# Performance work log

Measured on AMD Instinct MI355X. Metric: run time of the kernel, lower is better.

Reference implementation:

```python
import jax, jax.numpy as jnp
import numpy as np

B, S, I, C, P = 64, 14, 32, 10, 4   # batch, spatial, in-caps/pos, classes, pose size
ROUTINGS = 3
EPS = 1e-9


def setup_inputs() -> dict:
    key = jax.random.key(0)
    k1, k2, k3, k4, k5 = jax.random.split(key, 5)
    return {
        "inputs_pose": jax.random.normal(k1, (B, S, S, I, P, P), jnp.float32),
        "inputs_activation": jax.random.uniform(k2, (B, S, S, I), jnp.float32),
        "w": jax.random.normal(k3, (1, I, C, P, P), jnp.float32),
        "beta_v": jax.random.normal(k4, (1, C), jnp.float32) * 0.1,
        "beta_a": jax.random.normal(k5, (1, C), jnp.float32) * 0.1,
    }


def _em_routing(votes, i_act, beta_v, beta_a, routings):
    # votes: [B, N, C, 16], i_act: [B, N]
    Bn, N, Cc, D = votes.shape
    rr = jnp.full((Bn, N, Cc, 1), 1.0 / Cc, votes.dtype)  # uniform init assignments
    bv = beta_v.reshape(1, 1, Cc, 1)
    ba = beta_a.reshape(1, 1, Cc, 1)
    it_min, it_max = 1.0, min(float(routings), 3.0)  # inverse-temperature schedule
    o_mean = o_act = None
    for it in range(routings):
        inv_temp = it_min + (it_max - it_min) * it / max(1.0, routings - 1.0)
        # --- M step ---
        rr_p = rr * i_act[:, :, None, None]                        # [B,N,C,1]
        rr_sum = jnp.sum(rr_p, axis=1, keepdims=True)              # [B,1,C,1]
        o_mean = jnp.sum(rr_p * votes, axis=1, keepdims=True) / rr_sum   # [B,1,C,16]
        o_var = jnp.sum(rr_p * jnp.square(votes - o_mean), axis=1, keepdims=True) / rr_sum
        o_stdv = jnp.sqrt(o_var)                                   # [B,1,C,16]
        cost = jnp.sum((bv + jnp.log(o_stdv + EPS)) * rr_sum, axis=-1, keepdims=True)  # [B,1,C,1]
        o_act = jax.nn.sigmoid(inv_temp * (ba - cost))             # [B,1,C,1]
        # --- E step (skipped on last iteration) ---
        if it < routings - 1:
            logp = (-jnp.sum(jnp.square(votes - o_mean) / (2.0 * jnp.square(o_stdv) + EPS),
                             axis=-1, keepdims=True)
                    - jnp.sum(jnp.log(o_stdv + EPS), axis=-1, keepdims=True))  # [B,N,C,1]
            zz = jnp.log(o_act + EPS) + logp
            rr = jax.nn.softmax(zz, axis=2)
    return o_mean[:, 0], o_act[:, 0, :, 0]  # [B,C,16], [B,C]


def reference(inputs_pose, inputs_activation, w, beta_v, beta_a):
    # mat_transform: votes[b,h,w,i,c] = pose[b,h,w,i] @ W[i,c]   (4x4 matmuls)
    votes = jnp.einsum('bhwipq,icqr->bhwicpr', inputs_pose, w[0])
    votes = votes.reshape(B, S, S, I, C, P * P)
    # coordinate addition: scaled (row+0.5)/S onto pose element 0, col onto element 1
    coord = (jnp.arange(S, dtype=votes.dtype) + 0.5) / S
    votes = votes.at[..., 0].add(coord[None, :, None, None, None])
    votes = votes.at[..., 1].add(coord[None, None, :, None, None])
    votes = votes.reshape(B, S * S * I, C, P * P)
    acts = inputs_activation.reshape(B, S * S * I)
    o_mean, o_act = _em_routing(votes, acts, beta_v, beta_a, ROUTINGS)
    pose = o_mean.reshape(B, C, P, P)
    return pose, o_act
```

## Files before the change

kernel.cpp:

```cpp
#include <hip/hip_runtime.h>
#include <math.h>

#define Bsz 64
#define Ssz 14
#define Isz 32
#define Csz 10
#define Dsz 16
#define Nsz (Ssz*Ssz*Isz)
#define EPSF 1e-9f

#define CH   640
#define NCH  10
#define MCH  3136
#define PST  36
#define MST  72

template<int CTRL, int RMASK>
__device__ __forceinline__ float dpp_add(float x) {
    int y = __builtin_amdgcn_update_dpp(0, __float_as_int(x), CTRL, RMASK, 0xf, true);
    return x + __int_as_float(y);
}
__device__ __forceinline__ float wave_sum64(float x) {
    x = dpp_add<0x111, 0xf>(x);
    x = dpp_add<0x112, 0xf>(x);
    x = dpp_add<0x114, 0xf>(x);
    x = dpp_add<0x118, 0xf>(x);
    x = dpp_add<0x142, 0xa>(x);
    x = dpp_add<0x143, 0xc>(x);
    return x;
}

__global__ __launch_bounds__(640) void mom_kernel(
    const float* __restrict__ pose,
    const float* __restrict__ act,
    float* __restrict__ partM)
{
    const int b = blockIdx.x, mch = blockIdx.y;
    const int tid = threadIdx.x, lane = tid & 63;

    __shared__ float Macc[32][73];

    float s[69];
#pragma unroll
    for (int j = 0; j < 69; ++j) s[j] = 0.f;

    const float* poseb = pose + (size_t)b*Nsz*Dsz;
    const float* actb  = act  + (size_t)b*Nsz;
    const int base = mch*MCH;

    for (int k = 0; k < MCH; k += 640) {
        const int nl = k + tid;
        if (nl < MCH) {
            const int n = base + nl;
            const float4* pp = reinterpret_cast<const float4*>(poseb + (size_t)n*Dsz);
            float4 a0 = pp[0], a1 = pp[1], a2 = pp[2], a3 = pp[3];
            float p[16] = {a0.x,a0.y,a0.z,a0.w, a1.x,a1.y,a1.z,a1.w,
                           a2.x,a2.y,a2.z,a2.w, a3.x,a3.y,a3.z,a3.w};
            const int hw = n >> 5;
            const int wc = hw % Ssz, hr = hw / Ssz;
            const float chh = (hr+0.5f)*(1.0f/Ssz), cww = (wc+0.5f)*(1.0f/Ssz);
            const float wgt = actb[n]*(1.0f/Csz);
            s[0] += wgt;
            float wp[16];
#pragma unroll
            for (int j = 0; j < 16; ++j) { wp[j] = wgt*p[j]; s[1+j] += wp[j]; }
            int t = 17;
#pragma unroll
            for (int pr = 0; pr < 4; ++pr)
#pragma unroll
                for (int k1 = 0; k1 < 4; ++k1)
#pragma unroll
                    for (int k2 = k1; k2 < 4; ++k2)
                        s[t++] += wp[pr*4+k1]*p[pr*4+k2];
            const float wch = wgt*chh, wcw = wgt*cww;
#pragma unroll
            for (int j = 0; j < 4; ++j) { s[57+j] += wch*p[j]; s[61+j] += wcw*p[j]; }
            s[65] += wch; s[66] += wcw; s[67] += wch*chh; s[68] += wcw*cww;
        }
    }
#pragma unroll
    for (int j = 0; j < 69; ++j) s[j] += __shfl_xor(s[j], 32);

    for (int t = tid; t < 32*73; t += 640) (&Macc[0][0])[t] = 0.f;
    __syncthreads();
    if (lane < 32) {
#pragma unroll
        for (int j = 0; j < 69; ++j) atomicAdd(&Macc[lane][j], s[j]);
    }
    __syncthreads();
    float* ob = partM + (size_t)(b*2 + mch)*32*MST;
    for (int t = tid; t < 32*MST; t += 640) {
        const int i = t / MST, j = t - i*MST;
        ob[t] = (j < 69) ? Macc[i][j] : 0.f;
    }
}

__global__ __launch_bounds__(256) void fin0_kernel(
    const float* __restrict__ partM,
    const float* __restrict__ w,
    const float* __restrict__ beta_v, const float* __restrict__ beta_a,
    float* __restrict__ prm, float inv_temp)
{
    const int b = blockIdx.x, tid = threadIdx.x;
    __shared__ float Mr[32][73];
    __shared__ float Ws[Isz*Csz*Dsz];
    __shared__ float pm[Csz][16], pg[Csz][16], pl[Csz][16];
    __shared__ float s0sh;

    const float* p0 = partM + (size_t)(b*2 + 0)*32*MST;
    const float* p1 = partM + (size_t)(b*2 + 1)*32*MST;
    for (int t = tid; t < 32*MST; t += 256) {
        const int i = t / MST, j = t - i*MST;
        Mr[i][j] = p0[t] + p1[t];
    }
    for (int t = tid; t < Isz*Csz*Dsz; t += 256) Ws[t] = w[t];
    __syncthreads();

    if (tid < Csz*Dsz) {
        const int c = tid >> 4, d = tid & 15, pr = d >> 2, r = d & 3;
        float S0 = 0.f, S1 = 0.f, S2 = 0.f;
        for (int i = 0; i < 32; ++i) {
            const float* Wi = Ws + (i*Csz + c)*Dsz;
            const float* Mi = Mr[i];
            S0 += Mi[0];
            const float w0 = Wi[0*4+r], w1 = Wi[1*4+r], w2 = Wi[2*4+r], w3 = Wi[3*4+r];
            const float* M1 = Mi + 1 + pr*4;
            S1 += w0*M1[0] + w1*M1[1] + w2*M1[2] + w3*M1[3];
            const float* Q = Mi + 17 + pr*10;
            S2 += w0*w0*Q[0] + w1*w1*Q[4] + w2*w2*Q[7] + w3*w3*Q[9]
                + 2.f*(w0*w1*Q[1] + w0*w2*Q[2] + w0*w3*Q[3]
                     + w1*w2*Q[5] + w1*w3*Q[6] + w2*w3*Q[8]);
            if (d == 0) {
                S1 += Mi[65];
                S2 += 2.f*(w0*Mi[57] + w1*Mi[58] + w2*Mi[59] + w3*Mi[60]) + Mi[67];
            } else if (d == 1) {
                S1 += Mi[66];
                S2 += 2.f*(w0*Mi[61] + w1*Mi[62] + w2*Mi[63] + w3*Mi[64]) + Mi[68];
            }
        }
        const float mean = S1 / S0;
        const float var = fmaxf(S2/S0 - mean*mean, 0.f);
        pm[c][d] = mean;
        pg[c][d] = 1.f/(2.f*var + EPSF);
        pl[c][d] = __logf(sqrtf(var) + EPSF);
        if (tid == 0) s0sh = S0;
    }
    __syncthreads();
    if (tid < Csz) {
        const int c = tid;
        float sumlog = 0.f;
#pragma unroll
        for (int d = 0; d < 16; ++d) sumlog += pl[c][d];
        const float cost = s0sh*(16.f*beta_v[c] + sumlog);
        const float oact = 1.f/(1.f + __expf(-inv_temp*(beta_a[c] - cost)));
        const float K = __logf(oact + EPSF) - sumlog;
        float* o = prm + (size_t)(b*Csz + c)*PST;
#pragma unroll
        for (int d = 0; d < 16; ++d) { o[d] = pm[c][d]; o[16+d] = pg[c][d]; }
        o[32] = K;
    }
}

__global__ __launch_bounds__(640) void em_kernel(
    const float* __restrict__ pose, const float* __restrict__ act,
    const float* __restrict__ w, const float* __restrict__ prm,
    float* __restrict__ partC)
{
    const int b = blockIdx.x, chunk = blockIdx.y;
    const int tid = threadIdx.x, wv = tid >> 6, lane = tid & 63;

    __shared__ float Wm[Csz][Isz*17];
    __shared__ float rr[Csz][CH];

    for (int t = tid; t < Csz*Isz*Dsz; t += 640) {
        const int cc = t >> 9, rem = t & 511, i = rem >> 4, q = rem & 15;
        Wm[cc][i*17 + q] = w[(i*Csz + cc)*Dsz + q];
    }
    __syncthreads();

    const int base = chunk*CH;
    const float* poseb = pose + (size_t)b*Nsz*Dsz;

    {
        const int n = base + tid;
        if (n < Nsz) {
            const float4* pp = reinterpret_cast<const float4*>(poseb + (size_t)n*Dsz);
            float4 a0 = pp[0], a1 = pp[1], a2 = pp[2], a3 = pp[3];
            float p[16] = {a0.x,a0.y,a0.z,a0.w, a1.x,a1.y,a1.z,a1.w,
                           a2.x,a2.y,a2.z,a2.w, a3.x,a3.y,a3.z,a3.w};
            const int i = tid & 31;
            const int hw = n >> 5;
            const int wc = hw % Ssz, hr = hw / Ssz;
            const float chh = (hr+0.5f)*(1.0f/Ssz), cww = (wc+0.5f)*(1.0f/Ssz);
            const float a = act[(size_t)b*Nsz + n];
            float zz[Csz];
#pragma unroll
            for (int c = 0; c < Csz; ++c) {
                const float* __restrict__ Wi = &Wm[c][i*17];
                const float* __restrict__ pg = prm + (size_t)(b*Csz + c)*PST;
                float quad = 0.f;
#pragma unroll
                for (int pr = 0; pr < 4; ++pr) {
#pragma unroll
                    for (int r = 0; r < 4; ++r) {
                        float vv = p[pr*4+0]*Wi[0*4+r] + p[pr*4+1]*Wi[1*4+r]
                                 + p[pr*4+2]*Wi[2*4+r] + p[pr*4+3]*Wi[3*4+r];
                        if (pr == 0 && r == 0) vv += chh;
                        if (pr == 0 && r == 1) vv += cww;
                        const int d = pr*4 + r;
                        const float dv = vv - pg[d];
                        quad += dv*dv*pg[16+d];
                    }
                }
                zz[c] = pg[32] - quad;
            }
            float zmax = zz[0];
#pragma unroll
            for (int c = 1; c < Csz; ++c) zmax = fmaxf(zmax, zz[c]);
            float zsum = 0.f;
#pragma unroll
            for (int c = 0; c < Csz; ++c) { zz[c] = __expf(zz[c] - zmax); zsum += zz[c]; }
            const float sc = __fdividef(a, zsum);
#pragma unroll
            for (int c = 0; c < Csz; ++c) rr[c][tid] = zz[c]*sc;
        }
    }
    __syncthreads();

    const int c = wv;
    float W16[16];
#pragma unroll
    for (int j = 0; j < 16; ++j) W16[j] = Wm[c][(lane & 31)*17 + j];

    float s0 = 0.f, s1[16], s2[16];
#pragma unroll
    for (int d = 0; d < 16; ++d) { s1[d] = 0.f; s2[d] = 0.f; }

    for (int k = 0; k < CH; k += 64) {
        const int nl = k + lane;
        const int n = base + nl;
        if (n < Nsz) {
            const float4* pp = reinterpret_cast<const float4*>(poseb + (size_t)n*Dsz);
            const int hw = n >> 5;
            const int wc2 = hw % Ssz, hr2 = hw / Ssz;
            const float chh = (hr2+0.5f)*(1.0f/Ssz), cww = (wc2+0.5f)*(1.0f/Ssz);
            const float wgt = rr[c][nl];
            s0 += wgt;
#pragma unroll
            for (int pr = 0; pr < 4; ++pr) {
                const float4 pv = pp[pr];
#pragma unroll
                for (int r = 0; r < 4; ++r) {
                    float vv = pv.x*W16[0*4+r] + pv.y*W16[1*4+r]
                             + pv.z*W16[2*4+r] + pv.w*W16[3*4+r];
                    if (pr == 0 && r == 0) vv += chh;
                    if (pr == 0 && r == 1) vv += cww;
                    const float wvv = wgt*vv;
                    s1[pr*4+r] += wvv;
                    s2[pr*4+r] += wvv*vv;
                }
            }
        }
    }
    s0 = wave_sum64(s0);
#pragma unroll
    for (int d = 0; d < 16; ++d) { s1[d] = wave_sum64(s1[d]); s2[d] = wave_sum64(s2[d]); }
    if (lane == 63) {
        const int bc = b*Csz + c;
        float* pt = partC + (size_t)chunk*33*(Bsz*Csz) + bc;
        pt[0] = s0;
#pragma unroll
        for (int d = 0; d < 16; ++d) {
            pt[(size_t)(1+d)*(Bsz*Csz)]  = s1[d];
            pt[(size_t)(17+d)*(Bsz*Csz)] = s2[d];
        }
    }
}

__global__ __launch_bounds__(64) void fin12_kernel(
    const float* __restrict__ partC, const float* __restrict__ beta_v,
    const float* __restrict__ beta_a, float* __restrict__ prm,
    float* __restrict__ out, float inv_temp)
{
    const int bc = blockIdx.x*64 + threadIdx.x;
    const int c = bc % Csz;
    float S[33];
#pragma unroll
    for (int j = 0; j < 33; ++j) S[j] = 0.f;
    for (int ch = 0; ch < NCH; ++ch) {
        const float* pb = partC + (size_t)ch*33*(Bsz*Csz) + bc;
#pragma unroll
        for (int j = 0; j < 33; ++j) S[j] += pb[(size_t)j*(Bsz*Csz)];
    }
    const float S0 = S[0], rS0 = 1.f/S0;
    float mean[16], gv[16];
    float sumlog = 0.f;
#pragma unroll
    for (int d = 0; d < 16; ++d) {
        const float mn = S[1+d]*rS0;
        const float var = fmaxf(S[17+d]*rS0 - mn*mn, 0.f);
        mean[d] = mn;
        gv[d] = 1.f/(2.f*var + EPSF);
        sumlog += __logf(sqrtf(var) + EPSF);
    }
    const float cost = S0*(16.f*beta_v[c] + sumlog);
    const float oact = 1.f/(1.f + __expf(-inv_temp*(beta_a[c] - cost)));
    if (out) {
#pragma unroll
        for (int d = 0; d < 16; ++d) out[(size_t)bc*16 + d] = mean[d];
        out[(size_t)Bsz*Csz*Dsz + bc] = oact;
    } else {
        const float K = __logf(oact + EPSF) - sumlog;
        float* o = prm + (size_t)bc*PST;
#pragma unroll
        for (int d = 0; d < 16; ++d) { o[d] = mean[d]; o[16+d] = gv[d]; }
        o[32] = K;
    }
}

extern "C" void kernel_launch(void* const* d_in, const int* in_sizes, int n_in,
                              void* d_out, int out_size, void* d_ws, size_t ws_size,
                              hipStream_t stream)
{
    const float* pose = (const float*)d_in[0];
    const float* act  = (const float*)d_in[1];
    const float* w    = (const float*)d_in[2];
    const float* bv   = (const float*)d_in[3];
    const float* ba   = (const float*)d_in[4];
    float* out = (float*)d_out;

    float* partM = (float*)d_ws;
    float* partC = partM;
    float* prmA  = partM + (size_t)Bsz*2*32*MST;
    float* prmB  = prmA + (size_t)Bsz*Csz*PST;

    mom_kernel  <<<dim3(Bsz, 2),   640, 0, stream>>>(pose, act, partM);
    fin0_kernel <<<Bsz,            256, 0, stream>>>(partM, w, bv, ba, prmA, 1.0f);
    em_kernel   <<<dim3(Bsz, NCH), 640, 0, stream>>>(pose, act, w, prmA, partC);
    fin12_kernel<<<(Bsz*Csz)/64,    64, 0, stream>>>(partC, bv, ba, prmB, nullptr, 2.0f);
    em_kernel   <<<dim3(Bsz, NCH), 640, 0, stream>>>(pose, act, w, prmB, partC);
    fin12_kernel<<<(Bsz*Csz)/64,    64, 0, stream>>>(partC, bv, ba, nullptr, out, 3.0f);
}
```

Baseline: 254.7 us.

## Fuse finalize steps into EM kernels and restructure E-step per class wave

Removes the separate fin0 and intermediate fin12 kernels by having each EM block recompute the per-(batch, class) parameters from the partial moments at its start. mom_kernel now atomically accumulates its two halves into a zeroed buffer, which needs an extra memset. The E-step is restructured so each wave handles one class with its W in registers and the parameters broadcast via readlane, writing logits to shared memory before a per-point softmax pass. Every block redundantly redoes the reduction and the parameter math, and the launch bounds raise the occupancy target, which may pressure registers.

```diff
diff --git a/kernel.cpp b/kernel.cpp
--- a/kernel.cpp
+++ b/kernel.cpp
@@ -12,8 +12,9 @@
 #define CH   640
 #define NCH  10
 #define MCH  3136
-#define PST  36
-#define MST  72
+#define MROW 72
+#define PRMS 36
+#define BC   (Bsz*Csz)
 
 template<int CTRL, int RMASK>
 __device__ __forceinline__ float dpp_add(float x) {
@@ -56,10 +57,9 @@
             float4 a0 = pp[0], a1 = pp[1], a2 = pp[2], a3 = pp[3];
             float p[16] = {a0.x,a0.y,a0.z,a0.w, a1.x,a1.y,a1.z,a1.w,
                            a2.x,a2.y,a2.z,a2.w, a3.x,a3.y,a3.z,a3.w};
-            const int hw = n >> 5;
-            const int wc = hw % Ssz, hr = hw / Ssz;
-            const float chh = (hr+0.5f)*(1.0f/Ssz), cww = (wc+0.5f)*(1.0f/Ssz);
-            const float wgt = actb[n]*(1.0f/Csz);
+            const int hw = n >> 5, wc = hw % Ssz, hr = hw / Ssz;
+            const float chh = (hr+0.5f)*(1.f/Ssz), cww = (wc+0.5f)*(1.f/Ssz);
+            const float wgt = actb[n]*(1.f/Csz);
             s[0] += wgt;
             float wp[16];
 #pragma unroll
@@ -88,176 +88,195 @@
         for (int j = 0; j < 69; ++j) atomicAdd(&Macc[lane][j], s[j]);
     }
     __syncthreads();
-    float* ob = partM + (size_t)(b*2 + mch)*32*MST;
-    for (int t = tid; t < 32*MST; t += 640) {
-        const int i = t / MST, j = t - i*MST;
-        ob[t] = (j < 69) ? Macc[i][j] : 0.f;
-    }
-}
-
-__global__ __launch_bounds__(256) void fin0_kernel(
-    const float* __restrict__ partM,
-    const float* __restrict__ w,
-    const float* __restrict__ beta_v, const float* __restrict__ beta_a,
-    float* __restrict__ prm, float inv_temp)
-{
-    const int b = blockIdx.x, tid = threadIdx.x;
-    __shared__ float Mr[32][73];
-    __shared__ float Ws[Isz*Csz*Dsz];
-    __shared__ float pm[Csz][16], pg[Csz][16], pl[Csz][16];
-    __shared__ float s0sh;
-
-    const float* p0 = partM + (size_t)(b*2 + 0)*32*MST;
-    const float* p1 = partM + (size_t)(b*2 + 1)*32*MST;
-    for (int t = tid; t < 32*MST; t += 256) {
-        const int i = t / MST, j = t - i*MST;
-        Mr[i][j] = p0[t] + p1[t];
-    }
-    for (int t = tid; t < Isz*Csz*Dsz; t += 256) Ws[t] = w[t];
-    __syncthreads();
-
-    if (tid < Csz*Dsz) {
-        const int c = tid >> 4, d = tid & 15, pr = d >> 2, r = d & 3;
-        float S0 = 0.f, S1 = 0.f, S2 = 0.f;
-        for (int i = 0; i < 32; ++i) {
-            const float* Wi = Ws + (i*Csz + c)*Dsz;
-            const float* Mi = Mr[i];
-            S0 += Mi[0];
-            const float w0 = Wi[0*4+r], w1 = Wi[1*4+r], w2 = Wi[2*4+r], w3 = Wi[3*4+r];
-            const float* M1 = Mi + 1 + pr*4;
-            S1 += w0*M1[0] + w1*M1[1] + w2*M1[2] + w3*M1[3];
-            const float* Q = Mi + 17 + pr*10;
-            S2 += w0*w0*Q[0] + w1*w1*Q[4] + w2*w2*Q[7] + w3*w3*Q[9]
-                + 2.f*(w0*w1*Q[1] + w0*w2*Q[2] + w0*w3*Q[3]
-                     + w1*w2*Q[5] + w1*w3*Q[6] + w2*w3*Q[8]);
-            if (d == 0) {
-                S1 += Mi[65];
-                S2 += 2.f*(w0*Mi[57] + w1*Mi[58] + w2*Mi[59] + w3*Mi[60]) + Mi[67];
-            } else if (d == 1) {
-                S1 += Mi[66];
-                S2 += 2.f*(w0*Mi[61] + w1*Mi[62] + w2*Mi[63] + w3*Mi[64]) + Mi[68];
-            }
-        }
-        const float mean = S1 / S0;
-        const float var = fmaxf(S2/S0 - mean*mean, 0.f);
-        pm[c][d] = mean;
-        pg[c][d] = 1.f/(2.f*var + EPSF);
-        pl[c][d] = __logf(sqrtf(var) + EPSF);
-        if (tid == 0) s0sh = S0;
-    }
-    __syncthreads();
-    if (tid < Csz) {
-        const int c = tid;
-        float sumlog = 0.f;
-#pragma unroll
-        for (int d = 0; d < 16; ++d) sumlog += pl[c][d];
-        const float cost = s0sh*(16.f*beta_v[c] + sumlog);
-        const float oact = 1.f/(1.f + __expf(-inv_temp*(beta_a[c] - cost)));
-        const float K = __logf(oact + EPSF) - sumlog;
-        float* o = prm + (size_t)(b*Csz + c)*PST;
-#pragma unroll
-        for (int d = 0; d < 16; ++d) { o[d] = pm[c][d]; o[16+d] = pg[c][d]; }
-        o[32] = K;
-    }
-}
-
-__global__ __launch_bounds__(640) void em_kernel(
+    for (int t = tid; t < 32*MROW; t += 640) {
+        const int i = t / MROW, j = t - i*MROW;
+        if (j < 69) atomicAdd(&partM[(size_t)b*(32*MROW) + t], Macc[i][j]);
+    }
+}
+
+template<bool FIRST>
+__global__ __launch_bounds__(640, 5) void em_kernel(
     const float* __restrict__ pose, const float* __restrict__ act,
-    const float* __restrict__ w, const float* __restrict__ prm,
-    float* __restrict__ partC)
+    const float* __restrict__ w, const float* __restrict__ beta_v,
+    const float* __restrict__ beta_a, const float* __restrict__ partIn,
+    float* __restrict__ partOut, float inv_temp_prev)
 {
     const int b = blockIdx.x, chunk = blockIdx.y;
-    const int tid = threadIdx.x, wv = tid >> 6, lane = tid & 63;
-
-    __shared__ float Wm[Csz][Isz*17];
-    __shared__ float rr[Csz][CH];
-
-    for (int t = tid; t < Csz*Isz*Dsz; t += 640) {
-        const int cc = t >> 9, rem = t & 511, i = rem >> 4, q = rem & 15;
-        Wm[cc][i*17 + q] = w[(i*Csz + cc)*Dsz + q];
-    }
-    __syncthreads();
+    const int tid = threadIdx.x, wv_ = tid >> 6, lane = tid & 63;
+
+    __shared__ float Wm[FIRST ? Csz*Isz*17 : 1];
+    __shared__ float U2[Csz*CH];
+    __shared__ float prm[Csz][PRMS];
+    __shared__ float pl[Csz*Dsz];
+    __shared__ float s0sh;
+
+    if (FIRST) {
+        for (int t = tid; t < Csz*Isz*Dsz; t += 640) {
+            const int cc = t >> 9, rem = t & 511, i = rem >> 4, q = rem & 15;
+            Wm[cc*(Isz*17) + i*17 + q] = w[(i*Csz + cc)*Dsz + q];
+        }
+        for (int t = tid; t < 32*MROW; t += 640) {
+            const int i = t / MROW, j = t - i*MROW;
+            U2[i*73 + j] = partIn[(size_t)b*(32*MROW) + t];
+        }
+    } else {
+        if (tid < Csz*33) {
+            const int c2 = tid / 33, j = tid - c2*33;
+            float sacc = 0.f;
+            const float* pb = partIn + (size_t)j*BC + b*Csz + c2;
+            for (int ch = 0; ch < NCH; ++ch) sacc += pb[(size_t)ch*33*BC];
+            U2[c2*34 + j] = sacc;
+        }
+    }
+    __syncthreads();
+
+    if (tid < Csz*Dsz) {
+        const int c = tid >> 4, d = tid & 15;
+        if (FIRST) {
+            const int pr = d >> 2, r = d & 3;
+            float S0 = 0.f, S1 = 0.f, S2 = 0.f;
+            for (int i = 0; i < 32; ++i) {
+                const float* Mi = U2 + i*73;
+                const float* Wi = Wm + c*(Isz*17) + i*17;
+                S0 += Mi[0];
+                const float w0 = Wi[r], w1 = Wi[4+r], w2 = Wi[8+r], w3 = Wi[12+r];
+                const float* M1 = Mi + 1 + pr*4;
+                S1 += w0*M1[0] + w1*M1[1] + w2*M1[2] + w3*M1[3];
+                const float* Q = Mi + 17 + pr*10;
+                S2 += w0*w0*Q[0] + w1*w1*Q[4] + w2*w2*Q[7] + w3*w3*Q[9]
+                    + 2.f*(w0*w1*Q[1] + w0*w2*Q[2] + w0*w3*Q[3]
+                         + w1*w2*Q[5] + w1*w3*Q[6] + w2*w3*Q[8]);
+                if (d == 0) {
+                    S1 += Mi[65];
+                    S2 += 2.f*(w0*Mi[57] + w1*Mi[58] + w2*Mi[59] + w3*Mi[60]) + Mi[67];
+                } else if (d == 1) {
+                    S1 += Mi[66];
+                    S2 += 2.f*(w0*Mi[61] + w1*Mi[62] + w2*Mi[63] + w3*Mi[64]) + Mi[68];
+                }
+            }
+            const float mean = S1 / S0;
+            const float var = fmaxf(S2/S0 - mean*mean, 0.f);
+            prm[c][d]    = mean;
+            prm[c][16+d] = 1.f/(2.f*var + EPSF);
+            pl[tid]      = __logf(sqrtf(var) + EPSF);
+            if (tid == 0) s0sh = S0;
+        } else {
+            const float S0 = U2[c*34];
+            const float mn = U2[c*34 + 1 + d] / S0;
+            const float var = fmaxf(U2[c*34 + 17 + d]/S0 - mn*mn, 0.f);
+            prm[c][d]    = mn;
+            prm[c][16+d] = 1.f/(2.f*var + EPSF);
+            pl[tid]      = __logf(sqrtf(var) + EPSF);
+        }
+    }
+    __syncthreads();
+    if (tid < Csz) {
+        float sumlog = 0.f;
+#pragma unroll
+        for (int d = 0; d < 16; ++d) sumlog += pl[tid*16 + d];
+        const float S0 = FIRST ? s0sh : U2[tid*34];
+        const float cost = S0*(16.f*beta_v[tid] + sumlog);
+        const float oact = 1.f/(1.f + __expf(-inv_temp_prev*(beta_a[tid] - cost)));
+        prm[tid][32] = __logf(oact + EPSF) - sumlog;
+    }
+    __syncthreads();
+
+    const int c = wv_;
+    float W16[16];
+    if (FIRST) {
+#pragma unroll
+        for (int j = 0; j < 16; ++j) W16[j] = Wm[c*(Isz*17) + (lane & 31)*17 + j];
+    } else {
+        const float4* wp = reinterpret_cast<const float4*>(
+            w + ((size_t)(lane & 31)*Csz + c)*Dsz);
+        float4 q0 = wp[0], q1 = wp[1], q2 = wp[2], q3 = wp[3];
+        W16[0]=q0.x; W16[1]=q0.y; W16[2]=q0.z; W16[3]=q0.w;
+        W16[4]=q1.x; W16[5]=q1.y; W16[6]=q1.z; W16[7]=q1.w;
+        W16[8]=q2.x; W16[9]=q2.y; W16[10]=q2.z; W16[11]=q2.w;
+        W16[12]=q3.x; W16[13]=q3.y; W16[14]=q3.z; W16[15]=q3.w;
+    }
+    const float pv = (lane < 33) ? prm[c][lane] : 0.f;
+    const int pvi = __float_as_int(pv);
+    float m_s[16], g_s[16];
+#pragma unroll
+    for (int d = 0; d < 16; ++d) {
+        m_s[d] = __int_as_float(__builtin_amdgcn_readlane(pvi, d));
+        g_s[d] = __int_as_float(__builtin_amdgcn_readlane(pvi, 16 + d));
+    }
+    const float K_s = __int_as_float(__builtin_amdgcn_readlane(pvi, 32));
 
     const int base = chunk*CH;
     const float* poseb = pose + (size_t)b*Nsz*Dsz;
 
-    {
-        const int n = base + tid;
+    for (int k = 0; k < CH; k += 64) {
+        const int n = base + k + lane;
         if (n < Nsz) {
             const float4* pp = reinterpret_cast<const float4*>(poseb + (size_t)n*Dsz);
             float4 a0 = pp[0], a1 = pp[1], a2 = pp[2], a3 = pp[3];
             float p[16] = {a0.x,a0.y,a0.z,a0.w, a1.x,a1.y,a1.z,a1.w,
                            a2.x,a2.y,a2.z,a2.w, a3.x,a3.y,a3.z,a3.w};
-            const int i = tid & 31;
-            const int hw = n >> 5;
-            const int wc = hw % Ssz, hr = hw / Ssz;
-            const float chh = (hr+0.5f)*(1.0f/Ssz), cww = (wc+0.5f)*(1.0f/Ssz);
-            const float a = act[(size_t)b*Nsz + n];
-            float zz[Csz];
-#pragma unroll
-            for (int c = 0; c < Csz; ++c) {
-                const float* __restrict__ Wi = &Wm[c][i*17];
-                const float* __restrict__ pg = prm + (size_t)(b*Csz + c)*PST;
-                float quad = 0.f;
-#pragma unroll
-                for (int pr = 0; pr < 4; ++pr) {
-#pragma unroll
-                    for (int r = 0; r < 4; ++r) {
-                        float vv = p[pr*4+0]*Wi[0*4+r] + p[pr*4+1]*Wi[1*4+r]
-                                 + p[pr*4+2]*Wi[2*4+r] + p[pr*4+3]*Wi[3*4+r];
-                        if (pr == 0 && r == 0) vv += chh;
-                        if (pr == 0 && r == 1) vv += cww;
-                        const int d = pr*4 + r;
-                        const float dv = vv - pg[d];
-                        quad += dv*dv*pg[16+d];
-                    }
+            const int hw = n >> 5, wc2 = hw % Ssz, hr2 = hw / Ssz;
+            const float chh = (hr2+0.5f)*(1.f/Ssz), cww = (wc2+0.5f)*(1.f/Ssz);
+            float quad = 0.f;
+#pragma unroll
+            for (int pr = 0; pr < 4; ++pr) {
+#pragma unroll
+                for (int r = 0; r < 4; ++r) {
+                    float vvv = p[pr*4]*W16[r] + p[pr*4+1]*W16[4+r]
+                              + p[pr*4+2]*W16[8+r] + p[pr*4+3]*W16[12+r];
+                    if (pr == 0 && r == 0) vvv += chh;
+                    if (pr == 0 && r == 1) vvv += cww;
+                    const float dv = vvv - m_s[pr*4+r];
+                    quad += dv*dv*g_s[pr*4+r];
                 }
-                zz[c] = pg[32] - quad;
             }
-            float zmax = zz[0];
-#pragma unroll
-            for (int c = 1; c < Csz; ++c) zmax = fmaxf(zmax, zz[c]);
+            U2[c*CH + k + lane] = K_s - quad;
+        }
+    }
+    __syncthreads();
+
+    {
+        const int n = base + tid;
+        if (n < Nsz) {
+            float z[Csz];
+#pragma unroll
+            for (int cc = 0; cc < Csz; ++cc) z[cc] = U2[cc*CH + tid];
+            float zmax = z[0];
+#pragma unroll
+            for (int cc = 1; cc < Csz; ++cc) zmax = fmaxf(zmax, z[cc]);
             float zsum = 0.f;
 #pragma unroll
-            for (int c = 0; c < Csz; ++c) { zz[c] = __expf(zz[c] - zmax); zsum += zz[c]; }
-            const float sc = __fdividef(a, zsum);
-#pragma unroll
-            for (int c = 0; c < Csz; ++c) rr[c][tid] = zz[c]*sc;
-        }
-    }
-    __syncthreads();
-
-    const int c = wv;
-    float W16[16];
-#pragma unroll
-    for (int j = 0; j < 16; ++j) W16[j] = Wm[c][(lane & 31)*17 + j];
+            for (int cc = 0; cc < Csz; ++cc) { z[cc] = __expf(z[cc] - zmax); zsum += z[cc]; }
+            const float sc = __fdividef(act[(size_t)b*Nsz + n], zsum);
+#pragma unroll
+            for (int cc = 0; cc < Csz; ++cc) U2[cc*CH + tid] = z[cc]*sc;
+        }
+    }
+    __syncthreads();
 
     float s0 = 0.f, s1[16], s2[16];
 #pragma unroll
     for (int d = 0; d < 16; ++d) { s1[d] = 0.f; s2[d] = 0.f; }
-
     for (int k = 0; k < CH; k += 64) {
-        const int nl = k + lane;
-        const int n = base + nl;
+        const int n = base + k + lane;
         if (n < Nsz) {
             const float4* pp = reinterpret_cast<const float4*>(poseb + (size_t)n*Dsz);
-            const int hw = n >> 5;
-            const int wc2 = hw % Ssz, hr2 = hw / Ssz;
-            const float chh = (hr2+0.5f)*(1.0f/Ssz), cww = (wc2+0.5f)*(1.0f/Ssz);
-            const float wgt = rr[c][nl];
+            const int hw = n >> 5, wc2 = hw % Ssz, hr2 = hw / Ssz;
+            const float chh = (hr2+0.5f)*(1.f/Ssz), cww = (wc2+0.5f)*(1.f/Ssz);
+            const float wgt = U2[c*CH + k + lane];
             s0 += wgt;
 #pragma unroll
             for (int pr = 0; pr < 4; ++pr) {
-                const float4 pv = pp[pr];
+                const float4 pvv = pp[pr];
 #pragma unroll
                 for (int r = 0; r < 4; ++r) {
-                    float vv = pv.x*W16[0*4+r] + pv.y*W16[1*4+r]
-                             + pv.z*W16[2*4+r] + pv.w*W16[3*4+r];
-                    if (pr == 0 && r == 0) vv += chh;
-                    if (pr == 0 && r == 1) vv += cww;
-                    const float wvv = wgt*vv;
+                    float vvv = pvv.x*W16[r] + pvv.y*W16[4+r]
+                              + pvv.z*W16[8+r] + pvv.w*W16[12+r];
+                    if (pr == 0 && r == 0) vvv += chh;
+                    if (pr == 0 && r == 1) vvv += cww;
+                    const float wvv = wgt*vvv;
                     s1[pr*4+r] += wvv;
-                    s2[pr*4+r] += wvv*vv;
+                    s2[pr*4+r] += wvv*vvv;
                 }
             }
         }
@@ -266,21 +285,19 @@
 #pragma unroll
     for (int d = 0; d < 16; ++d) { s1[d] = wave_sum64(s1[d]); s2[d] = wave_sum64(s2[d]); }
     if (lane == 63) {
-        const int bc = b*Csz + c;
-        float* pt = partC + (size_t)chunk*33*(Bsz*Csz) + bc;
+        float* pt = partOut + (size_t)chunk*33*BC + b*Csz + c;
         pt[0] = s0;
 #pragma unroll
         for (int d = 0; d < 16; ++d) {
-            pt[(size_t)(1+d)*(Bsz*Csz)]  = s1[d];
-            pt[(size_t)(17+d)*(Bsz*Csz)] = s2[d];
-        }
-    }
-}
-
-__global__ __launch_bounds__(64) void fin12_kernel(
+            pt[(size_t)(1+d)*BC]  = s1[d];
+            pt[(size_t)(17+d)*BC] = s2[d];
+        }
+    }
+}
+
+__global__ __launch_bounds__(64) void fin_kernel(
     const float* __restrict__ partC, const float* __restrict__ beta_v,
-    const float* __restrict__ beta_a, float* __restrict__ prm,
-    float* __restrict__ out, float inv_temp)
+    const float* __restrict__ beta_a, float* __restrict__ out, float inv_temp)
 {
     const int bc = blockIdx.x*64 + threadIdx.x;
     const int c = bc % Csz;
@@ -288,40 +305,28 @@
 #pragma unroll
     for (int j = 0; j < 33; ++j) S[j] = 0.f;
     for (int ch = 0; ch < NCH; ++ch) {
-        const float* pb = partC + (size_t)ch*33*(Bsz*Csz) + bc;
-#pragma unroll
-        for (int j = 0; j < 33; ++j) S[j] += pb[(size_t)j*(Bsz*Csz)];
+        const float* pb = partC + (size_t)ch*33*BC + bc;
+#pragma unroll
+        for (int j = 0; j < 33; ++j) S[j] += pb[(size_t)j*BC];
     }
     const float S0 = S[0], rS0 = 1.f/S0;
-    float mean[16], gv[16];
     float sumlog = 0.f;
 #pragma unroll
     for (int d = 0; d < 16; ++d) {
         const float mn = S[1+d]*rS0;
         const float var = fmaxf(S[17+d]*rS0 - mn*mn, 0.f);
-        mean[d] = mn;
-        gv[d] = 1.f/(2.f*var + EPSF);
+        out[(size_t)bc*Dsz + d] = mn;
         sumlog += __logf(sqrtf(var) + EPSF);
     }
     const float cost = S0*(16.f*beta_v[c] + sumlog);
-    const float oact = 1.f/(1.f + __expf(-inv_temp*(beta_a[c] - cost)));
-    if (out) {
-#pragma unroll
-        for (int d = 0; d < 16; ++d) out[(size_t)bc*16 + d] = mean[d];
-        out[(size_t)Bsz*Csz*Dsz + bc] = oact;
-    } else {
-        const float K = __logf(oact + EPSF) - sumlog;
-        float* o = prm + (size_t)bc*PST;
-#pragma unroll
-        for (int d = 0; d < 16; ++d) { o[d] = mean[d]; o[16+d] = gv[d]; }
-        o[32] = K;
-    }
+    out[(size_t)Bsz*Csz*Dsz + bc] = 1.f/(1.f + __expf(-inv_temp*(beta_a[c] - cost)));
 }
 
 extern "C" void kernel_launch(void* const* d_in, const int* in_sizes, int n_in,
                               void* d_out, int out_size, void* d_ws, size_t ws_size,
                               hipStream_t stream)
 {
+    (void)in_sizes; (void)n_in; (void)out_size; (void)ws_size;
     const float* pose = (const float*)d_in[0];
     const float* act  = (const float*)d_in[1];
     const float* w    = (const float*)d_in[2];
@@ -329,15 +334,15 @@
     const float* ba   = (const float*)d_in[4];
     float* out = (float*)d_out;
 
-    float* partM = (float*)d_ws;
-    float* partC = partM;
-    float* prmA  = partM + (size_t)Bsz*2*32*MST;
-    float* prmB  = prmA + (size_t)Bsz*Csz*PST;
-
-    mom_kernel  <<<dim3(Bsz, 2),   640, 0, stream>>>(pose, act, partM);
-    fin0_kernel <<<Bsz,            256, 0, stream>>>(partM, w, bv, ba, prmA, 1.0f);
-    em_kernel   <<<dim3(Bsz, NCH), 640, 0, stream>>>(pose, act, w, prmA, partC);
-    fin12_kernel<<<(Bsz*Csz)/64,    64, 0, stream>>>(partC, bv, ba, prmB, nullptr, 2.0f);
-    em_kernel   <<<dim3(Bsz, NCH), 640, 0, stream>>>(pose, act, w, prmB, partC);
-    fin12_kernel<<<(Bsz*Csz)/64,    64, 0, stream>>>(partC, bv, ba, nullptr, out, 3.0f);
-}
+    float* regA = (float*)d_ws;
+    float* regB = regA + (size_t)NCH*33*BC;
+    float* partM  = regA;
+    float* partC  = regB;
+    float* partC2 = regA;
+
+    hipMemsetAsync(partM, 0, (size_t)Bsz*32*MROW*sizeof(float), stream);
+    mom_kernel      <<<dim3(Bsz, 2),   640, 0, stream>>>(pose, act, partM);
+    em_kernel<true> <<<dim3(Bsz, NCH), 640, 0, stream>>>(pose, act, w, bv, ba, partM, partC, 1.0f);
+    em_kernel<false><<<dim3(Bsz, NCH), 640, 0, stream>>>(pose, act, w, bv, ba, partC, partC2, 2.0f);
+    fin_kernel      <<<NCH,             64, 0, stream>>>(partC2, bv, ba, out, 3.0f);
+}
```

Measured after the change: 277.0 us. +8.8%, slower.

## Fuse moment accumulation with first M-step and parallelize finalize kernels

Applied to the files above, without the earlier changes.

Merges the moment-accumulation kernel and the first M-step finalize into one kernel per batch, which removes a launch and the partM round trip through global memory. The grid shrinks from 128 to 64 blocks, so each block now scans all N positions. The finalize kernel is reworked to run one 64-thread block per (batch, class), with the partial sums laid out contiguously per (b,c), so each thread reduces one statistic across the chunks and a shuffle reduction forms the log-sum. The trade-off is lower parallelism in the first kernel, which on a 256-CU part may lengthen that phase in exchange for the saved launch.

```diff
diff --git a/kernel.cpp b/kernel.cpp
--- a/kernel.cpp
+++ b/kernel.cpp
@@ -11,9 +11,9 @@
 
 #define CH   640
 #define NCH  10
-#define MCH  3136
 #define PST  36
-#define MST  72
+#define BC   (Bsz*Csz)
+#define CPL  (BC*33)
 
 template<int CTRL, int RMASK>
 __device__ __forceinline__ float dpp_add(float x) {
@@ -30,100 +30,80 @@
     return x;
 }
 
-__global__ __launch_bounds__(640) void mom_kernel(
+__global__ __launch_bounds__(640, 3) void momfin0_kernel(
     const float* __restrict__ pose,
     const float* __restrict__ act,
-    float* __restrict__ partM)
+    const float* __restrict__ w,
+    const float* __restrict__ beta_v,
+    const float* __restrict__ beta_a,
+    float* __restrict__ prmOut)
 {
-    const int b = blockIdx.x, mch = blockIdx.y;
+    const int b = blockIdx.x;
     const int tid = threadIdx.x, lane = tid & 63;
 
     __shared__ float Macc[32][73];
-
-    float s[69];
-#pragma unroll
-    for (int j = 0; j < 69; ++j) s[j] = 0.f;
+    __shared__ float U[3*640];
+    __shared__ float pl[Csz*Dsz];
+    __shared__ float sv[Csz];
+
+    for (int t = tid; t < 32*73; t += 640) (&Macc[0][0])[t] = 0.f;
+    __syncthreads();
 
     const float* poseb = pose + (size_t)b*Nsz*Dsz;
     const float* actb  = act  + (size_t)b*Nsz;
-    const int base = mch*MCH;
-
-    for (int k = 0; k < MCH; k += 640) {
-        const int nl = k + tid;
-        if (nl < MCH) {
-            const int n = base + nl;
-            const float4* pp = reinterpret_cast<const float4*>(poseb + (size_t)n*Dsz);
-            float4 a0 = pp[0], a1 = pp[1], a2 = pp[2], a3 = pp[3];
-            float p[16] = {a0.x,a0.y,a0.z,a0.w, a1.x,a1.y,a1.z,a1.w,
-                           a2.x,a2.y,a2.z,a2.w, a3.x,a3.y,a3.z,a3.w};
-            const int hw = n >> 5;
-            const int wc = hw % Ssz, hr = hw / Ssz;
-            const float chh = (hr+0.5f)*(1.0f/Ssz), cww = (wc+0.5f)*(1.0f/Ssz);
-            const float wgt = actb[n]*(1.0f/Csz);
-            s[0] += wgt;
-            float wp[16];
-#pragma unroll
-            for (int j = 0; j < 16; ++j) { wp[j] = wgt*p[j]; s[1+j] += wp[j]; }
-            int t = 17;
-#pragma unroll
-            for (int pr = 0; pr < 4; ++pr)
-#pragma unroll
-                for (int k1 = 0; k1 < 4; ++k1)
-#pragma unroll
-                    for (int k2 = k1; k2 < 4; ++k2)
-                        s[t++] += wp[pr*4+k1]*p[pr*4+k2];
-            const float wch = wgt*chh, wcw = wgt*cww;
-#pragma unroll
-            for (int j = 0; j < 4; ++j) { s[57+j] += wch*p[j]; s[61+j] += wcw*p[j]; }
-            s[65] += wch; s[66] += wcw; s[67] += wch*chh; s[68] += wcw*cww;
-        }
-    }
-#pragma unroll
-    for (int j = 0; j < 69; ++j) s[j] += __shfl_xor(s[j], 32);
-
-    for (int t = tid; t < 32*73; t += 640) (&Macc[0][0])[t] = 0.f;
+
+    {
+        float s[69];
+#pragma unroll
+        for (int j = 0; j < 69; ++j) s[j] = 0.f;
+        for (int k = 0; k < Nsz; k += CH) {
+            const int n = k + tid;
+            if (n < Nsz) {
+                const float4* pp = reinterpret_cast<const float4*>(poseb + (size_t)n*Dsz);
+                float4 a0 = pp[0], a1 = pp[1], a2 = pp[2], a3 = pp[3];
+                float p[16] = {a0.x,a0.y,a0.z,a0.w, a1.x,a1.y,a1.z,a1.w,
+                               a2.x,a2.y,a2.z,a2.w, a3.x,a3.y,a3.z,a3.w};
+                const int hw = n >> 5, wc = hw % Ssz, hr = hw / Ssz;
+                const float chh = (hr+0.5f)*(1.f/Ssz), cww = (wc+0.5f)*(1.f/Ssz);
+                const float wgt = actb[n]*(1.f/Csz);
+                s[0] += wgt;
+                float wp[16];
+#pragma unroll
+                for (int j = 0; j < 16; ++j) { wp[j] = wgt*p[j]; s[1+j] += wp[j]; }
+                int t = 17;
+#pragma unroll
+                for (int pr = 0; pr < 4; ++pr)
+#pragma unroll
+                    for (int k1 = 0; k1 < 4; ++k1)
+#pragma unroll
+                        for (int k2 = k1; k2 < 4; ++k2)
+                            s[t++] += wp[pr*4+k1]*p[pr*4+k2];
+                const float wch = wgt*chh, wcw = wgt*cww;
+#pragma unroll
+                for (int j = 0; j < 4; ++j) { s[57+j] += wch*p[j]; s[61+j] += wcw*p[j]; }
+                s[65] += wch; s[66] += wcw; s[67] += wch*chh; s[68] += wcw*cww;
+            }
+        }
+#pragma unroll
+        for (int j = 0; j < 69; ++j) s[j] += __shfl_xor(s[j], 32);
+        if (lane < 32) {
+#pragma unroll
+            for (int j = 0; j < 69; ++j) atomicAdd(&Macc[lane][j], s[j]);
+        }
+    }
     __syncthreads();
-    if (lane < 32) {
-#pragma unroll
-        for (int j = 0; j < 69; ++j) atomicAdd(&Macc[lane][j], s[j]);
-    }
-    __syncthreads();
-    float* ob = partM + (size_t)(b*2 + mch)*32*MST;
-    for (int t = tid; t < 32*MST; t += 640) {
-        const int i = t / MST, j = t - i*MST;
-        ob[t] = (j < 69) ? Macc[i][j] : 0.f;
-    }
-}
-
-__global__ __launch_bounds__(256) void fin0_kernel(
-    const float* __restrict__ partM,
-    const float* __restrict__ w,
-    const float* __restrict__ beta_v, const float* __restrict__ beta_a,
-    float* __restrict__ prm, float inv_temp)
-{
-    const int b = blockIdx.x, tid = threadIdx.x;
-    __shared__ float Mr[32][73];
-    __shared__ float Ws[Isz*Csz*Dsz];
-    __shared__ float pm[Csz][16], pg[Csz][16], pl[Csz][16];
-    __shared__ float s0sh;
-
-    const float* p0 = partM + (size_t)(b*2 + 0)*32*MST;
-    const float* p1 = partM + (size_t)(b*2 + 1)*32*MST;
-    for (int t = tid; t < 32*MST; t += 256) {
-        const int i = t / MST, j = t - i*MST;
-        Mr[i][j] = p0[t] + p1[t];
-    }
-    for (int t = tid; t < Isz*Csz*Dsz; t += 256) Ws[t] = w[t];
-    __syncthreads();
-
-    if (tid < Csz*Dsz) {
-        const int c = tid >> 4, d = tid & 15, pr = d >> 2, r = d & 3;
+
+    {
+        const int c = tid >> 6, d = (tid >> 2) & 15, g = tid & 3;
+        const int pr = d >> 2, r = d & 3;
         float S0 = 0.f, S1 = 0.f, S2 = 0.f;
-        for (int i = 0; i < 32; ++i) {
-            const float* Wi = Ws + (i*Csz + c)*Dsz;
-            const float* Mi = Mr[i];
+#pragma unroll
+        for (int ii = 0; ii < 8; ++ii) {
+            const int i = g*8 + ii;
+            const float* Mi = Macc[i];
+            const float* Wi = w + ((size_t)i*Csz + c)*Dsz;
             S0 += Mi[0];
-            const float w0 = Wi[0*4+r], w1 = Wi[1*4+r], w2 = Wi[2*4+r], w3 = Wi[3*4+r];
+            const float w0 = Wi[r], w1 = Wi[4+r], w2 = Wi[8+r], w3 = Wi[12+r];
             const float* M1 = Mi + 1 + pr*4;
             S1 += w0*M1[0] + w1*M1[1] + w2*M1[2] + w3*M1[3];
             const float* Q = Mi + 17 + pr*10;
@@ -138,26 +118,31 @@
                 S2 += 2.f*(w0*Mi[61] + w1*Mi[62] + w2*Mi[63] + w3*Mi[64]) + Mi[68];
             }
         }
-        const float mean = S1 / S0;
-        const float var = fmaxf(S2/S0 - mean*mean, 0.f);
-        pm[c][d] = mean;
-        pg[c][d] = 1.f/(2.f*var + EPSF);
-        pl[c][d] = __logf(sqrtf(var) + EPSF);
-        if (tid == 0) s0sh = S0;
-    }
-    __syncthreads();
-    if (tid < Csz) {
-        const int c = tid;
-        float sumlog = 0.f;
-#pragma unroll
-        for (int d = 0; d < 16; ++d) sumlog += pl[c][d];
-        const float cost = s0sh*(16.f*beta_v[c] + sumlog);
-        const float oact = 1.f/(1.f + __expf(-inv_temp*(beta_a[c] - cost)));
-        const float K = __logf(oact + EPSF) - sumlog;
-        float* o = prm + (size_t)(b*Csz + c)*PST;
-#pragma unroll
-        for (int d = 0; d < 16; ++d) { o[d] = pm[c][d]; o[16+d] = pg[c][d]; }
-        o[32] = K;
+        U[tid] = S0; U[640 + tid] = S1; U[1280 + tid] = S2;
+        __syncthreads();
+        if (g == 0) {
+            float T0 = 0.f, T1 = 0.f, T2 = 0.f;
+#pragma unroll
+            for (int kk = 0; kk < 4; ++kk) {
+                T0 += U[tid + kk]; T1 += U[640 + tid + kk]; T2 += U[1280 + tid + kk];
+            }
+            const float mean = T1 / T0;
+            const float var = fmaxf(T2/T0 - mean*mean, 0.f);
+            float* o = prmOut + (size_t)(b*Csz + c)*PST;
+            o[d]    = mean;
+            o[16+d] = 1.f/(2.f*var + EPSF);
+            pl[tid >> 2] = __logf(sqrtf(var) + EPSF);
+            if (d == 0) sv[c] = T0;
+        }
+        __syncthreads();
+        if (tid < Csz) {
+            float sumlog = 0.f;
+#pragma unroll
+            for (int d2 = 0; d2 < 16; ++d2) sumlog += pl[tid*16 + d2];
+            const float cost = sv[tid]*(16.f*beta_v[tid] + sumlog);
+            const float oact = 1.f/(1.f + __expf(-1.0f*(beta_a[tid] - cost)));
+            prmOut[(size_t)(b*Csz + tid)*PST + 32] = __logf(oact + EPSF) - sumlog;
+        }
     }
 }
 
@@ -266,55 +251,58 @@
 #pragma unroll
     for (int d = 0; d < 16; ++d) { s1[d] = wave_sum64(s1[d]); s2[d] = wave_sum64(s2[d]); }
     if (lane == 63) {
-        const int bc = b*Csz + c;
-        float* pt = partC + (size_t)chunk*33*(Bsz*Csz) + bc;
+        float* pt = partC + (size_t)chunk*CPL + (size_t)(b*Csz + c)*33;
         pt[0] = s0;
 #pragma unroll
-        for (int d = 0; d < 16; ++d) {
-            pt[(size_t)(1+d)*(Bsz*Csz)]  = s1[d];
-            pt[(size_t)(17+d)*(Bsz*Csz)] = s2[d];
-        }
-    }
-}
-
-__global__ __launch_bounds__(64) void fin12_kernel(
+        for (int d = 0; d < 16; ++d) { pt[1+d] = s1[d]; pt[17+d] = s2[d]; }
+    }
+}
+
+__global__ __launch_bounds__(64) void fin_kernel(
     const float* __restrict__ partC, const float* __restrict__ beta_v,
-    const float* __restrict__ beta_a, float* __restrict__ prm,
+    const float* __restrict__ beta_a, float* __restrict__ prmOut,
     float* __restrict__ out, float inv_temp)
 {
-    const int bc = blockIdx.x*64 + threadIdx.x;
+    const int bc = blockIdx.x;
     const int c = bc % Csz;
-    float S[33];
-#pragma unroll
-    for (int j = 0; j < 33; ++j) S[j] = 0.f;
-    for (int ch = 0; ch < NCH; ++ch) {
-        const float* pb = partC + (size_t)ch*33*(Bsz*Csz) + bc;
-#pragma unroll
-        for (int j = 0; j < 33; ++j) S[j] += pb[(size_t)j*(Bsz*Csz)];
-    }
-    const float S0 = S[0], rS0 = 1.f/S0;
-    float mean[16], gv[16];
-    float sumlog = 0.f;
-#pragma unroll
-    for (int d = 0; d < 16; ++d) {
-        const float mn = S[1+d]*rS0;
-        const float var = fmaxf(S[17+d]*rS0 - mn*mn, 0.f);
-        mean[d] = mn;
-        gv[d] = 1.f/(2.f*var + EPSF);
-        sumlog += __logf(sqrtf(var) + EPSF);
-    }
-    const float cost = S0*(16.f*beta_v[c] + sumlog);
-    const float oact = 1.f/(1.f + __expf(-inv_temp*(beta_a[c] - cost)));
+    const int j = threadIdx.x;
+
+    float S = 0.f;
+    if (j < 33) {
+        const float* pb = partC + (size_t)bc*33 + j;
+#pragma unroll
+        for (int ch = 0; ch < NCH; ++ch) S += pb[(size_t)ch*CPL];
+    }
+    const float S0 = __shfl(S, 0);
+    const float rS0 = 1.f / S0;
+
+    const int src = (j >= 1 && j <= 16) ? (16 + j) : 0;
+    const float S2d = __shfl(S, src);
+    float mn = 0.f, lg = 0.f, iv = 0.f;
+    if (j >= 1 && j <= 16) {
+        mn = S * rS0;
+        const float var = fmaxf(S2d * rS0 - mn*mn, 0.f);
+        iv = 1.f/(2.f*var + EPSF);
+        lg = __logf(sqrtf(var) + EPSF);
+    }
+    float sumlog = lg;
+#pragma unroll
+    for (int m = 32; m >= 1; m >>= 1) sumlog += __shfl_xor(sumlog, m);
+
     if (out) {
-#pragma unroll
-        for (int d = 0; d < 16; ++d) out[(size_t)bc*16 + d] = mean[d];
-        out[(size_t)Bsz*Csz*Dsz + bc] = oact;
+        if (j >= 1 && j <= 16) out[(size_t)bc*Dsz + (j-1)] = mn;
+        if (j == 0) {
+            const float cost = S0*(16.f*beta_v[c] + sumlog);
+            out[(size_t)Bsz*Csz*Dsz + bc] = 1.f/(1.f + __expf(-inv_temp*(beta_a[c] - cost)));
+        }
     } else {
-        const float K = __logf(oact + EPSF) - sumlog;
-        float* o = prm + (size_t)bc*PST;
-#pragma unroll
-        for (int d = 0; d < 16; ++d) { o[d] = mean[d]; o[16+d] = gv[d]; }
-        o[32] = K;
+        float* o = prmOut + (size_t)bc*PST;
+        if (j >= 1 && j <= 16) { o[j-1] = mn; o[16 + (j-1)] = iv; }
+        if (j == 0) {
+            const float cost = S0*(16.f*beta_v[c] + sumlog);
+            const float oact = 1.f/(1.f + __expf(-inv_temp*(beta_a[c] - cost)));
+            o[32] = __logf(oact + EPSF) - sumlog;
+        }
     }
 }
 
@@ -322,6 +310,7 @@
                               void* d_out, int out_size, void* d_ws, size_t ws_size,
                               hipStream_t stream)
 {
+    (void)in_sizes; (void)n_in; (void)out_size; (void)ws_size;
     const float* pose = (const float*)d_in[0];
     const float* act  = (const float*)d_in[1];
     const float* w    = (const float*)d_in[2];
@@ -329,15 +318,13 @@
     const float* ba   = (const float*)d_in[4];
     float* out = (float*)d_out;
 
-    float* partM = (float*)d_ws;
-    float* partC = partM;
-    float* prmA  = partM + (size_t)Bsz*2*32*MST;
-    float* prmB  = prmA + (size_t)Bsz*Csz*PST;
-
-    mom_kernel  <<<dim3(Bsz, 2),   640, 0, stream>>>(pose, act, partM);
-    fin0_kernel <<<Bsz,            256, 0, stream>>>(partM, w, bv, ba, prmA, 1.0f);
-    em_kernel   <<<dim3(Bsz, NCH), 640, 0, stream>>>(pose, act, w, prmA, partC);
-    fin12_kernel<<<(Bsz*Csz)/64,    64, 0, stream>>>(partC, bv, ba, prmB, nullptr, 2.0f);
-    em_kernel   <<<dim3(Bsz, NCH), 640, 0, stream>>>(pose, act, w, prmB, partC);
-    fin12_kernel<<<(Bsz*Csz)/64,    64, 0, stream>>>(partC, bv, ba, nullptr, out, 3.0f);
-}
+    float* partC = (float*)d_ws;
+    float* prmA  = partC + (size_t)NCH*CPL;
+    float* prmB  = prmA + (size_t)BC*PST;
+
+    momfin0_kernel<<<Bsz,             640, 0, stream>>>(pose, act, w, bv, ba, prmA);
+    em_kernel     <<<dim3(Bsz, NCH),  640, 0, stream>>>(pose, act, w, prmA, partC);
+    fin_kernel    <<<BC,               64, 0, stream>>>(partC, bv, ba, prmB, nullptr, 2.0f);
+    em_kernel     <<<dim3(Bsz, NCH),  640, 0, stream>>>(pose, act, w, prmB, partC);
+    fin_kernel    <<<BC,               64, 0, stream>>>(partC, bv, ba, nullptr, out, 3.0f);
+}
```

Result: slower. 261.3 us (+2.6%).
